# Optimization experiments

Measured on AMD Instinct MI355X. Metric: run time of the kernel, lower is better.

## Reference

```python
import jax, jax.numpy as jnp
import numpy as np

T = 8192        # total atoms in the batch
B = 256         # number of molecules
N_VOCAB = 10000 # fingerprint vocabulary size
DIM = 64
L_HIDDEN = 3
L_OUTPUT = 2
EPS = 1e-12     # F.normalize eps


def setup_inputs() -> dict:
    key = jax.random.key(0)
    ks = jax.random.split(key, 8)
    fingerprints = jax.random.randint(ks[0], (T,), 0, N_VOCAB)
    atoms_per_mol = T // B
    segment_ids = jnp.repeat(jnp.arange(B), atoms_per_mol)  # sorted, like torch.split
    # Block-diagonal padded adjacency: random bonds inside each molecule block,
    # exact zeros off the diagonal blocks (this is what self.pad() produces).
    block_mask = segment_ids[:, None] == segment_ids[None, :]
    bonds = (jax.random.uniform(ks[1], (T, T)) < 0.15).astype(jnp.float32)
    adjacency = jnp.where(block_mask, bonds, 0.0)
    embed = jax.random.normal(ks[2], (N_VOCAB, DIM), dtype=jnp.float32) * 0.02
    W_fp = jax.random.normal(ks[3], (L_HIDDEN, DIM, DIM), dtype=jnp.float32) * (DIM ** -0.5)
    b_fp = jnp.zeros((L_HIDDEN, DIM), dtype=jnp.float32)
    W_out = jax.random.normal(ks[4], (L_OUTPUT, DIM, DIM), dtype=jnp.float32) * (DIM ** -0.5)
    b_out = jnp.zeros((L_OUTPUT, DIM), dtype=jnp.float32)
    W_prop = jax.random.normal(ks[5], (1, DIM), dtype=jnp.float32) * (DIM ** -0.5)
    b_prop = jnp.zeros((1,), dtype=jnp.float32)
    return {
        "fingerprints": fingerprints, "adjacency": adjacency, "segment_ids": segment_ids,
        "embed": embed, "W_fp": W_fp, "b_fp": b_fp,
        "W_out": W_out, "b_out": b_out, "W_prop": W_prop, "b_prop": b_prop,
    }


def reference(fingerprints, adjacency, segment_ids, embed, W_fp, b_fp,
              W_out, b_out, W_prop, b_prop):
    # embedding lookup: [T, DIM]
    v = embed[fingerprints]
    # GNN layers: h = relu(Wx+b); v = l2norm(h + A @ h)
    for l in range(W_fp.shape[0]):
        h = jax.nn.relu(v @ W_fp[l].T + b_fp[l])
        hs = h + adjacency @ h
        norm = jnp.linalg.norm(hs, axis=1, keepdims=True)
        v = hs / jnp.maximum(norm, EPS)
    # molecular vectors: segment sum over atoms of each molecule -> [B, DIM]
    mol = jax.ops.segment_sum(v, segment_ids, num_segments=B)
    # output MLP
    for l in range(W_out.shape[0]):
        mol = jax.nn.relu(mol @ W_out[l].T + b_out[l])
    return mol @ W_prop.T + b_prop  # [B, 1] predicted property
```

## Files before the change

### kernel.cpp

```cpp
#include <hip/hip_runtime.h>

#define T_ATOMS 8192
#define NMOL 256
#define APM 32
#define DIM 64
#define LHID 3
#define LOUT 2
#define EPSN 1e-12f

__global__ __launch_bounds__(256) void mgnn_kernel(
    const int*   __restrict__ fingerprints,
    const float* __restrict__ adjacency,
    const float* __restrict__ embed,
    const float* __restrict__ W_fp,
    const float* __restrict__ b_fp,
    const float* __restrict__ W_out,
    const float* __restrict__ b_out,
    const float* __restrict__ W_prop,
    const float* __restrict__ b_prop,
    float*       __restrict__ out)
{
    __shared__ float sV[APM][DIM];
    __shared__ float sH[APM][DIM];
    __shared__ float sA[APM][APM];
    __shared__ float sWt[DIM][DIM + 1];
    __shared__ float sB[DIM];
    __shared__ float sMol[DIM];

    const int m    = blockIdx.x;
    const int tid  = threadIdx.x;
    const int lane = tid & 63;
    const int wave = tid >> 6;

    for (int idx = tid; idx < APM * DIM; idx += 256) {
        int a = idx >> 6;
        int d = idx & 63;
        int fp = fingerprints[m * APM + a];
        sV[a][d] = embed[(size_t)fp * DIM + d];
    }
    for (int idx = tid; idx < APM * APM; idx += 256) {
        int i = idx >> 5;
        int j = idx & 31;
        sA[i][j] = adjacency[(size_t)(m * APM + i) * T_ATOMS + (m * APM + j)];
    }

    for (int l = 0; l < LHID; ++l) {
        for (int idx = tid; idx < DIM * DIM; idx += 256) {
            int d = idx >> 6;
            int k = idx & 63;
            sWt[k][d] = W_fp[l * DIM * DIM + idx];
        }
        if (tid < DIM) sB[tid] = b_fp[l * DIM + tid];
        __syncthreads();

        float hreg[8];
        #pragma unroll
        for (int e = 0; e < 8; ++e) {
            int i = wave * 8 + e;
            float acc = sB[lane];
            #pragma unroll
            for (int k = 0; k < DIM; ++k)
                acc = fmaf(sV[i][k], sWt[k][lane], acc);
            hreg[e] = fmaxf(acc, 0.0f);
        }
        __syncthreads();
        #pragma unroll
        for (int e = 0; e < 8; ++e) sH[wave * 8 + e][lane] = hreg[e];
        __syncthreads();

        #pragma unroll
        for (int e = 0; e < 8; ++e) {
            int i = wave * 8 + e;
            float acc = hreg[e];
            #pragma unroll
            for (int j = 0; j < APM; ++j)
                acc = fmaf(sA[i][j], sH[j][lane], acc);
            float ss = acc * acc;
            #pragma unroll
            for (int off = 32; off > 0; off >>= 1)
                ss += __shfl_xor(ss, off, 64);
            float inv = 1.0f / fmaxf(sqrtf(ss), EPSN);
            sV[i][lane] = acc * inv;
        }
        __syncthreads();
    }

    if (tid < DIM) {
        float acc = 0.0f;
        #pragma unroll
        for (int i = 0; i < APM; ++i) acc += sV[i][tid];
        sMol[tid] = acc;
    }
    __syncthreads();

    for (int l = 0; l < LOUT; ++l) {
        float acc = 0.0f;
        if (tid < DIM) {
            acc = b_out[l * DIM + tid];
            #pragma unroll
            for (int k = 0; k < DIM; ++k)
                acc = fmaf(sMol[k], W_out[l * DIM * DIM + tid * DIM + k], acc);
            acc = fmaxf(acc, 0.0f);
        }
        __syncthreads();
        if (tid < DIM) sMol[tid] = acc;
        __syncthreads();
    }

    if (tid == 0) {
        float acc = b_prop[0];
        #pragma unroll
        for (int k = 0; k < DIM; ++k)
            acc = fmaf(sMol[k], W_prop[k], acc);
        out[m] = acc;
    }
}

extern "C" void kernel_launch(void* const* d_in, const int* in_sizes, int n_in,
                              void* d_out, int out_size, void* d_ws, size_t ws_size,
                              hipStream_t stream) {
    const int*   fingerprints = (const int*)  d_in[0];
    const float* adjacency    = (const float*)d_in[1];
    const float* embed        = (const float*)d_in[3];
    const float* W_fp         = (const float*)d_in[4];
    const float* b_fp         = (const float*)d_in[5];
    const float* W_out        = (const float*)d_in[6];
    const float* b_out        = (const float*)d_in[7];
    const float* W_prop       = (const float*)d_in[8];
    const float* b_prop       = (const float*)d_in[9];
    float* out = (float*)d_out;

    mgnn_kernel<<<NMOL, 256, 0, stream>>>(fingerprints, adjacency, embed,
                                          W_fp, b_fp, W_out, b_out,
                                          W_prop, b_prop, out);
}
```

Baseline: 343.9 us.

## Keep per-lane weight rows in registers, prefetch next layer, use 512 threads

Each lane now holds its row of W_fp in 16 float4 registers instead of staging a transposed weight tile in shared memory, and it prefetches the next layer's weights while the current layer computes. The block grows to 512 threads, so each wave handles 4 atoms instead of 8, and adjacency and weight reads are vectorised with float4. This drops the shared-memory weight staging and one barrier per layer and gives more waves per block. The cost is heavy register pressure (two 64-float weight buffers plus accumulators), which may limit occupancy or cause spills.

```diff
diff --git a/kernel.cpp b/kernel.cpp
--- a/kernel.cpp
+++ b/kernel.cpp
@@ -8,7 +8,7 @@
 #define LOUT 2
 #define EPSN 1e-12f
 
-__global__ __launch_bounds__(256) void mgnn_kernel(
+__global__ __launch_bounds__(512, 2) void mgnn_kernel(
     const int*   __restrict__ fingerprints,
     const float* __restrict__ adjacency,
     const float* __restrict__ embed,
@@ -23,64 +23,93 @@
     __shared__ float sV[APM][DIM];
     __shared__ float sH[APM][DIM];
     __shared__ float sA[APM][APM];
-    __shared__ float sWt[DIM][DIM + 1];
-    __shared__ float sB[DIM];
     __shared__ float sMol[DIM];
 
     const int m    = blockIdx.x;
     const int tid  = threadIdx.x;
     const int lane = tid & 63;
     const int wave = tid >> 6;
+    const int i0   = wave * 4;
 
-    for (int idx = tid; idx < APM * DIM; idx += 256) {
+    for (int idx = tid; idx < APM * DIM; idx += 512) {
         int a = idx >> 6;
         int d = idx & 63;
         int fp = fingerprints[m * APM + a];
         sV[a][d] = embed[(size_t)fp * DIM + d];
     }
-    for (int idx = tid; idx < APM * APM; idx += 256) {
-        int i = idx >> 5;
-        int j = idx & 31;
-        sA[i][j] = adjacency[(size_t)(m * APM + i) * T_ATOMS + (m * APM + j)];
+    if (tid < APM * APM / 4) {
+        int i = tid >> 3;
+        int jg = tid & 7;
+        const float* src = adjacency + (size_t)(m * APM + i) * T_ATOMS + m * APM;
+        *(float4*)&sA[i][jg * 4] = ((const float4*)src)[jg];
     }
 
+    const float4* Wv = (const float4*)W_fp;
+    float4 wcur[16];
+    #pragma unroll
+    for (int kg = 0; kg < 16; ++kg) wcur[kg] = Wv[lane * 16 + kg];
+
+    __syncthreads();
+
+    #pragma unroll
     for (int l = 0; l < LHID; ++l) {
-        for (int idx = tid; idx < DIM * DIM; idx += 256) {
-            int d = idx >> 6;
-            int k = idx & 63;
-            sWt[k][d] = W_fp[l * DIM * DIM + idx];
+        float bias = b_fp[l * DIM + lane];
+
+        float4 wnext[16];
+        if (l + 1 < LHID) {
+            #pragma unroll
+            for (int kg = 0; kg < 16; ++kg)
+                wnext[kg] = Wv[(l + 1) * 1024 + lane * 16 + kg];
         }
-        if (tid < DIM) sB[tid] = b_fp[l * DIM + tid];
-        __syncthreads();
 
-        float hreg[8];
+        float acc[4] = {bias, bias, bias, bias};
         #pragma unroll
-        for (int e = 0; e < 8; ++e) {
-            int i = wave * 8 + e;
-            float acc = sB[lane];
+        for (int kg = 0; kg < 16; ++kg) {
+            float4 wv = wcur[kg];
             #pragma unroll
-            for (int k = 0; k < DIM; ++k)
-                acc = fmaf(sV[i][k], sWt[k][lane], acc);
-            hreg[e] = fmaxf(acc, 0.0f);
+            for (int e = 0; e < 4; ++e) {
+                float4 vv = *(const float4*)&sV[i0 + e][kg * 4];
+                acc[e] = fmaf(vv.x, wv.x, acc[e]);
+                acc[e] = fmaf(vv.y, wv.y, acc[e]);
+                acc[e] = fmaf(vv.z, wv.z, acc[e]);
+                acc[e] = fmaf(vv.w, wv.w, acc[e]);
+            }
         }
-        __syncthreads();
         #pragma unroll
-        for (int e = 0; e < 8; ++e) sH[wave * 8 + e][lane] = hreg[e];
+        for (int e = 0; e < 4; ++e) {
+            acc[e] = fmaxf(acc[e], 0.0f);
+            sH[i0 + e][lane] = acc[e];
+        }
         __syncthreads();
 
         #pragma unroll
-        for (int e = 0; e < 8; ++e) {
-            int i = wave * 8 + e;
-            float acc = hreg[e];
+        for (int jg = 0; jg < 8; ++jg) {
+            float hj[4];
             #pragma unroll
-            for (int j = 0; j < APM; ++j)
-                acc = fmaf(sA[i][j], sH[j][lane], acc);
-            float ss = acc * acc;
+            for (int t = 0; t < 4; ++t) hj[t] = sH[jg * 4 + t][lane];
+            #pragma unroll
+            for (int e = 0; e < 4; ++e) {
+                float4 av = *(const float4*)&sA[i0 + e][jg * 4];
+                acc[e] = fmaf(av.x, hj[0], acc[e]);
+                acc[e] = fmaf(av.y, hj[1], acc[e]);
+                acc[e] = fmaf(av.z, hj[2], acc[e]);
+                acc[e] = fmaf(av.w, hj[3], acc[e]);
+            }
+        }
+
+        #pragma unroll
+        for (int e = 0; e < 4; ++e) {
+            float ss = acc[e] * acc[e];
             #pragma unroll
             for (int off = 32; off > 0; off >>= 1)
                 ss += __shfl_xor(ss, off, 64);
             float inv = 1.0f / fmaxf(sqrtf(ss), EPSN);
-            sV[i][lane] = acc * inv;
+            sV[i0 + e][lane] = acc[e] * inv;
+        }
+
+        if (l + 1 < LHID) {
+            #pragma unroll
+            for (int kg = 0; kg < 16; ++kg) wcur[kg] = wnext[kg];
         }
         __syncthreads();
     }
@@ -93,13 +122,21 @@
     }
     __syncthreads();
 
+    #pragma unroll
     for (int l = 0; l < LOUT; ++l) {
         float acc = 0.0f;
         if (tid < DIM) {
             acc = b_out[l * DIM + tid];
+            const float4* wo = (const float4*)(W_out + l * DIM * DIM + tid * DIM);
             #pragma unroll
-            for (int k = 0; k < DIM; ++k)
-                acc = fmaf(sMol[k], W_out[l * DIM * DIM + tid * DIM + k], acc);
+            for (int kg = 0; kg < 16; ++kg) {
+                float4 w4 = wo[kg];
+                float4 m4 = *(const float4*)&sMol[kg * 4];
+                acc = fmaf(m4.x, w4.x, acc);
+                acc = fmaf(m4.y, w4.y, acc);
+                acc = fmaf(m4.z, w4.z, acc);
+                acc = fmaf(m4.w, w4.w, acc);
+            }
             acc = fmaxf(acc, 0.0f);
         }
         __syncthreads();
@@ -110,8 +147,14 @@
     if (tid == 0) {
         float acc = b_prop[0];
         #pragma unroll
-        for (int k = 0; k < DIM; ++k)
-            acc = fmaf(sMol[k], W_prop[k], acc);
+        for (int kg = 0; kg < 16; ++kg) {
+            float4 w4 = ((const float4*)W_prop)[kg];
+            float4 m4 = *(const float4*)&sMol[kg * 4];
+            acc = fmaf(m4.x, w4.x, acc);
+            acc = fmaf(m4.y, w4.y, acc);
+            acc = fmaf(m4.z, w4.z, acc);
+            acc = fmaf(m4.w, w4.w, acc);
+        }
         out[m] = acc;
     }
 }
@@ -130,7 +173,7 @@
     const float* b_prop       = (const float*)d_in[9];
     float* out = (float*)d_out;
 
-    mgnn_kernel<<<NMOL, 256, 0, stream>>>(fingerprints, adjacency, embed,
+    mgnn_kernel<<<NMOL, 512, 0, stream>>>(fingerprints, adjacency, embed,
                                           W_fp, b_fp, W_out, b_out,
                                           W_prop, b_prop, out);
 }
```

Result: faster. 331.3 us (-3.7%).
